# Kernel tuning notes

Hardware: AMD Instinct MI355X
Metric: run time of the kernel (lower is better)

Reference implementation:

```python
import jax, jax.numpy as jnp
import numpy as np

N = 1024      # nodes
IN = 64       # input_dim
H = 128       # hidden_dim
L = 4         # num graph layers
HEADS = 4     # MHA heads


def setup_inputs() -> dict:
    key = jax.random.key(0)
    ks = jax.random.split(key, 12)
    s = lambda k, shape: (jax.random.normal(k, shape, dtype=jnp.float32) * 0.05)
    z = lambda shape: jnp.zeros(shape, jnp.float32)
    return {
        "x": jax.random.normal(ks[0], (N, IN), dtype=jnp.float32),
        "emb_W": s(ks[1], (IN, H)), "emb_b": z((H,)),
        "ln_g": jnp.ones((H,), jnp.float32), "ln_b": z((H,)),
        "edge_W1": s(ks[2], (2 * H, H)), "edge_b1": z((H,)),
        "edge_W2": s(ks[3], (H, 1)), "edge_b2": z((1,)),
        "gc_W": s(ks[4], (L, H, H)), "gc_b": z((L, H)),
        "in_proj_W": s(ks[5], (3 * H, H)), "in_proj_b": z((3 * H,)),
        "out_proj_W": s(ks[6], (H, H)), "out_proj_b": z((H,)),
        "out_W": s(ks[7], (H, 6)), "out_b": z((6,)),
    }


def reference(x, emb_W, emb_b, ln_g, ln_b, edge_W1, edge_b1, edge_W2, edge_b2,
              gc_W, gc_b, in_proj_W, in_proj_b, out_proj_W, out_proj_b,
              out_W, out_b):
    # node embedding: Linear -> LayerNorm -> ReLU
    h = x @ emb_W + emb_b
    mu = h.mean(-1, keepdims=True)
    var = ((h - mu) ** 2).mean(-1, keepdims=True)
    h = (h - mu) * jax.lax.rsqrt(var + 1e-5) * ln_g + ln_b
    h = jax.nn.relu(h)

    n, Hd = h.shape
    # dynamic graph: edge MLP on concat(x_i, x_j) for all pairs, batched.
    # cat([x_i, x_j]) @ W1 == x_i @ W1[:H] + x_j @ W1[H:]
    a = h @ edge_W1[:Hd]          # [n, H]
    b = h @ edge_W1[Hd:]          # [n, H]
    e = jax.nn.relu(a[:, None, :] + b[None, :, :] + edge_b1)   # [n, n, H]
    adj = jax.nn.sigmoid(jnp.einsum('ijh,ho->ijo', e, edge_W2)[..., 0] + edge_b2[0])
    adj = adj * (1.0 - jnp.eye(n, dtype=adj.dtype))             # no self-edges

    # physics-informed graph conv layers: adj @ (h @ W) + b
    for l in range(gc_W.shape[0]):
        h = adj @ (h @ gc_W[l]) + gc_b[l]

    # MultiheadAttention (self-attention, seq=n, batch=1)
    d = Hd // HEADS
    qkv = h @ in_proj_W.T + in_proj_b
    q, k, v = jnp.split(qkv, 3, axis=-1)
    q = q.reshape(n, HEADS, d).transpose(1, 0, 2)   # [h, n, d]
    k = k.reshape(n, HEADS, d).transpose(1, 0, 2)
    v = v.reshape(n, HEADS, d).transpose(1, 0, 2)
    scale = 1.0 / np.sqrt(d).astype(np.float32)
    attn = jax.nn.softmax(jnp.einsum('hnd,hmd->hnm', q, k) * scale, axis=-1)
    o = jnp.einsum('hnm,hmd->hnd', attn, v).transpose(1, 0, 2).reshape(n, Hd)
    h = o @ out_proj_W.T + out_proj_b

    # pooled head + per-metric activations
    out = h.mean(0) @ out_W + out_b                 # [6]
    sig = jax.nn.sigmoid(out)
    return jnp.stack([sig[0], jax.nn.relu(out[1]), sig[2], sig[3], sig[4], sig[5]])
```

## Files before the change

kernel.cpp:

```cpp
#include <hip/hip_runtime.h>
#include <math.h>

#define NN 1024
#define IN_DIM 64
#define H 128
#define NL 4
#define HEADS 4
#define DH 32
#define KSPLIT 8
#define NSPLIT 16

__global__ __launch_bounds__(128) void k_embed(const float* __restrict__ x,
        const float* __restrict__ embW, const float* __restrict__ embB,
        const float* __restrict__ lng, const float* __restrict__ lnb,
        const float* __restrict__ eW1, const float* __restrict__ eb1,
        const float* __restrict__ gcW0,
        const float* __restrict__ inW, const float* __restrict__ outW,
        float* __restrict__ Wt_in, float* __restrict__ Wt_out,
        float* __restrict__ aM, float* __restrict__ bM, float* __restrict__ g0) {
    __shared__ float xs[IN_DIM];
    __shared__ float hs[H];
    __shared__ float red[H];
    int i = blockIdx.x, t = threadIdx.x;
    int gidx = i * 128 + t;
    if (gidx < 49152) {
        Wt_in[gidx] = inW[(gidx % 384) * 128 + gidx / 384];
    } else if (gidx < 65536) {
        int i2 = gidx - 49152;
        Wt_out[i2] = outW[(i2 % 128) * 128 + i2 / 128];
    }
    if (t < IN_DIM) xs[t] = x[i * IN_DIM + t];
    __syncthreads();
    float acc = embB[t];
    #pragma unroll 8
    for (int k = 0; k < IN_DIM; ++k) acc = fmaf(xs[k], embW[k * H + t], acc);
    red[t] = acc; __syncthreads();
    for (int s = 64; s > 0; s >>= 1) { if (t < s) red[t] += red[t + s]; __syncthreads(); }
    float mu = red[0] * (1.f / H);
    __syncthreads();
    float d = acc - mu;
    red[t] = d * d; __syncthreads();
    for (int s = 64; s > 0; s >>= 1) { if (t < s) red[t] += red[t + s]; __syncthreads(); }
    float var = red[0] * (1.f / H);
    float hv = d * rsqrtf(var + 1e-5f) * lng[t] + lnb[t];
    hv = fmaxf(hv, 0.f);
    hs[t] = hv;
    __syncthreads();
    float aa = eb1[t], bb = 0.f, gg = 0.f;
    #pragma unroll 8
    for (int k = 0; k < H; ++k) {
        float hk = hs[k];
        aa = fmaf(hk, eW1[k * H + t], aa);
        bb = fmaf(hk, eW1[(H + k) * H + t], bb);
        gg = fmaf(hk, gcW0[k * H + t], gg);
    }
    aM[i * H + t] = aa;
    bM[i * H + t] = bb;
    g0[i * H + t] = gg;
}

#define AT 32
__global__ __launch_bounds__(256) void k_adj(const float* __restrict__ aM, const float* __restrict__ bM,
        const float* __restrict__ w2, const float* __restrict__ eb2p, float* __restrict__ adj) {
    __shared__ float as_[AT][H + 4];
    __shared__ float bst[H][AT + 4];
    __shared__ float w2s[H];
    int i0 = blockIdx.y * AT, j0 = blockIdx.x * AT;
    int t = threadIdx.x;
    for (int idx = t; idx < AT * H; idx += 256) {
        int r = idx >> 7, c = idx & 127;
        as_[r][c] = aM[(i0 + r) * H + c];
        bst[c][r] = bM[(j0 + r) * H + c];
    }
    if (t < H) w2s[t] = w2[t];
    __syncthreads();
    int ti = t >> 3, tjg = t & 7;
    float a0 = 0.f, a1 = 0.f, a2 = 0.f, a3 = 0.f;
    const float eb2 = eb2p[0];
    #pragma unroll 4
    for (int h = 0; h < H; ++h) {
        float av = as_[ti][h];
        float4 bv = *(const float4*)&bst[h][tjg * 4];
        float wh = w2s[h];
        a0 = fmaf(fmaxf(av + bv.x, 0.f), wh, a0);
        a1 = fmaf(fmaxf(av + bv.y, 0.f), wh, a1);
        a2 = fmaf(fmaxf(av + bv.z, 0.f), wh, a2);
        a3 = fmaf(fmaxf(av + bv.w, 0.f), wh, a3);
    }
    int i = i0 + ti, jb = j0 + tjg * 4;
    float4 ov;
    ov.x = (i == jb + 0) ? 0.f : 1.f / (1.f + __expf(-(a0 + eb2)));
    ov.y = (i == jb + 1) ? 0.f : 1.f / (1.f + __expf(-(a1 + eb2)));
    ov.z = (i == jb + 2) ? 0.f : 1.f / (1.f + __expf(-(a2 + eb2)));
    ov.w = (i == jb + 3) ? 0.f : 1.f / (1.f + __expf(-(a3 + eb2)));
    *(float4*)&adj[(size_t)i * NN + jb] = ov;
}

__global__ __launch_bounds__(128) void k_spmm(const float* __restrict__ adj, const float* __restrict__ g,
        float* __restrict__ partial) {
    __shared__ float adjs[16][65];
    int r0 = blockIdx.x * 16;
    int j0 = blockIdx.y * 64;
    int t = threadIdx.x;
    #pragma unroll
    for (int it = 0; it < 2; ++it) {
        int idx = t + it * 128;
        int r = idx >> 4, jg = idx & 15;
        float4 av = *(const float4*)&adj[(size_t)(r0 + r) * NN + j0 + jg * 4];
        adjs[r][jg * 4 + 0] = av.x; adjs[r][jg * 4 + 1] = av.y;
        adjs[r][jg * 4 + 2] = av.z; adjs[r][jg * 4 + 3] = av.w;
    }
    __syncthreads();
    int rg = t >> 5, cg = t & 31;
    int c0 = cg * 4;
    float acc[4][4] = {};
    #pragma unroll 4
    for (int jj = 0; jj < 64; ++jj) {
        float ga[4];
        *(float4*)ga = *(const float4*)&g[(j0 + jj) * H + c0];
        #pragma unroll
        for (int r = 0; r < 4; ++r) {
            float av = adjs[rg * 4 + r][jj];
            #pragma unroll
            for (int c = 0; c < 4; ++c) acc[r][c] = fmaf(av, ga[c], acc[r][c]);
        }
    }
    #pragma unroll
    for (int r = 0; r < 4; ++r) {
        float4 ov = {acc[r][0], acc[r][1], acc[r][2], acc[r][3]};
        *(float4*)&partial[((size_t)blockIdx.y * NN + r0 + rg * 4 + r) * H + c0] = ov;
    }
}

__global__ __launch_bounds__(128) void k_redmat128(const float* __restrict__ partial,
        const float* __restrict__ bias, const float* __restrict__ W, float* __restrict__ outM) {
    __shared__ float s[H];
    int i = blockIdx.x, t = threadIdx.x;
    float v = bias[t];
    #pragma unroll
    for (int p = 0; p < NSPLIT; ++p) v += partial[(size_t)p * NN * H + i * H + t];
    s[t] = v;
    __syncthreads();
    float acc = 0.f;
    #pragma unroll 8
    for (int k = 0; k < H; ++k) acc = fmaf(s[k], W[k * H + t], acc);
    outM[i * H + t] = acc;
}

__global__ __launch_bounds__(384) void k_redmat384(const float* __restrict__ partial,
        const float* __restrict__ bias, const float* __restrict__ W,
        const float* __restrict__ bias2, float* __restrict__ outM) {
    __shared__ float s[H];
    int i = blockIdx.x, t = threadIdx.x;
    if (t < H) {
        float v = bias[t];
        #pragma unroll
        for (int p = 0; p < NSPLIT; ++p) v += partial[(size_t)p * NN * H + i * H + t];
        s[t] = v;
    }
    __syncthreads();
    float acc = bias2[t];
    #pragma unroll 8
    for (int k = 0; k < H; ++k) acc = fmaf(s[k], W[k * 384 + t], acc);
    outM[i * 384 + t] = acc;
}

__global__ __launch_bounds__(256) void k_attn_part(const float* __restrict__ qkv,
        float* __restrict__ opart, float* __restrict__ mpart, float* __restrict__ lpart) {
    __shared__ float kob[4][32][36];
    __shared__ float qT[32][36];
    __shared__ float pT[128][36];
    __shared__ float marr[32], larr[32];
    float* kT = &kob[0][0][0];
    const int t = threadIdx.x;
    const int head = blockIdx.y, kp = blockIdx.z;
    const int i0 = blockIdx.x * 32, j0 = kp * 128;
    const int qoff = head * DH, koff = H + head * DH, voff = 2 * H + head * DH;
    const float scale = 0.17677669529663687f;
    {
        int qi = t >> 3, dg = t & 7;
        float4 qv = *(const float4*)&qkv[(i0 + qi) * 384 + qoff + dg * 4];
        qT[dg * 4 + 0][qi] = qv.x * scale;
        qT[dg * 4 + 1][qi] = qv.y * scale;
        qT[dg * 4 + 2][qi] = qv.z * scale;
        qT[dg * 4 + 3][qi] = qv.w * scale;
    }
    #pragma unroll
    for (int it = 0; it < 4; ++it) {
        int idx = t + it * 256;
        int j = idx >> 3, dg = idx & 7;
        float4 kv = *(const float4*)&qkv[(j0 + j) * 384 + koff + dg * 4];
        kT[(dg * 4 + 0) * 132 + j] = kv.x;
        kT[(dg * 4 + 1) * 132 + j] = kv.y;
        kT[(dg * 4 + 2) * 132 + j] = kv.z;
        kT[(dg * 4 + 3) * 132 + j] = kv.w;
    }
    __syncthreads();
    const int tq = t >> 5, tj = t & 31;
    float s[4][4] = {};
    #pragma unroll
    for (int kk = 0; kk < DH; ++kk) {
        float qa[4], ka[4];
        *(float4*)qa = *(float4*)&qT[kk][tq * 4];
        *(float4*)ka = *(float4*)&kT[kk * 132 + tj * 4];
        #pragma unroll
        for (int a = 0; a < 4; ++a)
            #pragma unroll
            for (int b = 0; b < 4; ++b) s[a][b] = fmaf(qa[a], ka[b], s[a][b]);
    }
    #pragma unroll
    for (int a = 0; a < 4; ++a) {
        float mm = fmaxf(fmaxf(s[a][0], s[a][1]), fmaxf(s[a][2], s[a][3]));
        #pragma unroll
        for (int off = 16; off > 0; off >>= 1) mm = fmaxf(mm, __shfl_xor(mm, off));
        float ll = 0.f;
        #pragma unroll
        for (int b = 0; b < 4; ++b) { s[a][b] = __expf(s[a][b] - mm); ll += s[a][b]; }
        #pragma unroll
        for (int off = 16; off > 0; off >>= 1) ll += __shfl_xor(ll, off);
        if (tj == 0) { marr[tq * 4 + a] = mm; larr[tq * 4 + a] = ll; }
    }
    #pragma unroll
    for (int b = 0; b < 4; ++b)
        #pragma unroll
        for (int a = 0; a < 4; ++a) pT[tj * 4 + b][tq * 4 + a] = s[a][b];
    __syncthreads();
    const int qg = t >> 5, dg = (t >> 2) & 7, st = t & 3;
    float o[4][4] = {};
    #pragma unroll 4
    for (int jj = 0; jj < 32; ++jj) {
        int j = st * 32 + jj;
        float pa[4], va[4];
        *(float4*)pa = *(float4*)&pT[j][qg * 4];
        *(float4*)va = *(const float4*)&qkv[(j0 + j) * 384 + voff + dg * 4];
        #pragma unroll
        for (int a = 0; a < 4; ++a)
            #pragma unroll
            for (int b = 0; b < 4; ++b) o[a][b] = fmaf(pa[a], va[b], o[a][b]);
    }
    #pragma unroll
    for (int a = 0; a < 4; ++a)
        #pragma unroll
        for (int b = 0; b < 4; ++b) kob[st][qg * 4 + a][dg * 4 + b] = o[a][b];
    __syncthreads();
    {
        int q = t >> 3, d0 = (t & 7) * 4;
        float r0[4], r1[4], r2[4], r3[4];
        *(float4*)r0 = *(float4*)&kob[0][q][d0];
        *(float4*)r1 = *(float4*)&kob[1][q][d0];
        *(float4*)r2 = *(float4*)&kob[2][q][d0];
        *(float4*)r3 = *(float4*)&kob[3][q][d0];
        float4 ov;
        ov.x = (r0[0] + r1[0]) + (r2[0] + r3[0]);
        ov.y = (r0[1] + r1[1]) + (r2[1] + r3[1]);
        ov.z = (r0[2] + r1[2]) + (r2[2] + r3[2]);
        ov.w = (r0[3] + r1[3]) + (r2[3] + r3[3]);
        int pidx = head * KSPLIT + kp;
        *(float4*)&opart[((size_t)pidx * NN + i0 + q) * DH + d0] = ov;
        if (t < 32) {
            mpart[pidx * NN + i0 + t] = marr[t];
            lpart[pidx * NN + i0 + t] = larr[t];
        }
    }
}

__global__ __launch_bounds__(128) void k_mergeproj(const float* __restrict__ opart,
        const float* __restrict__ mpart, const float* __restrict__ lpart,
        const float* __restrict__ Wt_out, const float* __restrict__ bias,
        float* __restrict__ h2) {
    __shared__ float s[H];
    int row = blockIdx.x, t = threadIdx.x;
    int head = t >> 5, d = t & 31;
    float mv[KSPLIT];
    float M = -1e30f;
    #pragma unroll
    for (int p = 0; p < KSPLIT; ++p) {
        mv[p] = mpart[(head * KSPLIT + p) * NN + row];
        M = fmaxf(M, mv[p]);
    }
    float L = 0.f, o = 0.f;
    #pragma unroll
    for (int p = 0; p < KSPLIT; ++p) {
        float w = __expf(mv[p] - M);
        L = fmaf(lpart[(head * KSPLIT + p) * NN + row], w, L);
        o = fmaf(opart[((size_t)(head * KSPLIT + p) * NN + row) * DH + d], w, o);
    }
    s[t] = o / L;
    __syncthreads();
    float acc = bias[t];
    #pragma unroll 8
    for (int k = 0; k < H; ++k) acc = fmaf(s[k], Wt_out[k * H + t], acc);
    h2[row * H + t] = acc;
}

__global__ void k_pool1(const float* __restrict__ h2, float* __restrict__ pp) {
    int b = blockIdx.x;
    int t = threadIdx.x;
    int c = t & 127, rg = t >> 7;
    int r0 = b * 32 + rg * 16;
    float s = 0.f;
    #pragma unroll
    for (int r = 0; r < 16; ++r) s += h2[(r0 + r) * H + c];
    pp[(b * 2 + rg) * H + c] = s;
}

__global__ void k_pool2(const float* __restrict__ pp, const float* __restrict__ outW,
        const float* __restrict__ outB, float* __restrict__ out) {
    __shared__ float pooled[H];
    int t = threadIdx.x;
    float s = 0.f;
    #pragma unroll 8
    for (int p = 0; p < 64; ++p) s += pp[p * H + t];
    pooled[t] = s * (1.f / 1024.f);
    __syncthreads();
    if (t < 6) {
        float acc = outB[t];
        for (int c = 0; c < H; ++c) acc = fmaf(pooled[c], outW[c * 6 + t], acc);
        out[t] = (t == 1) ? fmaxf(acc, 0.f) : 1.f / (1.f + expf(-acc));
    }
}

extern "C" void kernel_launch(void* const* d_in, const int* in_sizes, int n_in,
                              void* d_out, int out_size, void* d_ws, size_t ws_size,
                              hipStream_t stream) {
    const float* x       = (const float*)d_in[0];
    const float* emb_W   = (const float*)d_in[1];
    const float* emb_b   = (const float*)d_in[2];
    const float* ln_g    = (const float*)d_in[3];
    const float* ln_b    = (const float*)d_in[4];
    const float* edge_W1 = (const float*)d_in[5];
    const float* edge_b1 = (const float*)d_in[6];
    const float* edge_W2 = (const float*)d_in[7];
    const float* edge_b2 = (const float*)d_in[8];
    const float* gc_W    = (const float*)d_in[9];
    const float* gc_b    = (const float*)d_in[10];
    const float* in_proj_W  = (const float*)d_in[11];
    const float* in_proj_b  = (const float*)d_in[12];
    const float* out_proj_W = (const float*)d_in[13];
    const float* out_proj_b = (const float*)d_in[14];
    const float* out_W   = (const float*)d_in[15];
    const float* out_b   = (const float*)d_in[16];
    float* out = (float*)d_out;

    float* ws = (float*)d_ws;
    float* aM      = ws;
    float* bM      = aM + NN * H;
    float* adj     = bM + NN * H;
    float* g       = adj + NN * NN;
    float* partial = g + NN * H;
    float* qkv     = partial + (size_t)NSPLIT * NN * H;
    float* Wt_in   = qkv + NN * 384;
    float* Wt_out  = Wt_in + 128 * 384;
    float* pp      = Wt_out + 128 * 128;
    float* opart = adj;
    float* mpart = aM;
    float* lpart = aM + 32 * NN;
    float* h2    = g;

    k_embed<<<NN, 128, 0, stream>>>(x, emb_W, emb_b, ln_g, ln_b, edge_W1, edge_b1,
                                    gc_W, in_proj_W, out_proj_W, Wt_in, Wt_out,
                                    aM, bM, g);
    k_adj<<<dim3(NN / AT, NN / AT), 256, 0, stream>>>(aM, bM, edge_W2, edge_b2, adj);

    for (int l = 0; l < NL; ++l) {
        k_spmm<<<dim3(NN / 16, NSPLIT), 128, 0, stream>>>(adj, g, partial);
        if (l < NL - 1)
            k_redmat128<<<NN, 128, 0, stream>>>(partial, gc_b + (size_t)l * H,
                                                gc_W + (size_t)(l + 1) * H * H, g);
        else
            k_redmat384<<<NN, 384, 0, stream>>>(partial, gc_b + (size_t)l * H,
                                                Wt_in, in_proj_b, qkv);
    }

    k_attn_part<<<dim3(NN / 32, HEADS, KSPLIT), 256, 0, stream>>>(qkv, opart, mpart, lpart);
    k_mergeproj<<<NN, 128, 0, stream>>>(opart, mpart, lpart, Wt_out, out_proj_b, h2);
    k_pool1<<<32, 256, 0, stream>>>(h2, pp);
    k_pool2<<<1, 128, 0, stream>>>(pp, out_W, out_b, out);
}
```

Baseline: 159.3 us.

## Register-tile edge MLP kernel and batch multiple rows per block

The pairwise adjacency kernel moves to 64x64 output tiles. Each thread computes a 4x4 register block, and the hidden dimension is staged through transposed shared tiles in chunks of 32. This cuts shared-memory loads per FMA in the dominant N²·H edge computation. The embed and reduce-matmul kernels now handle four rows per block so each weight load is reused across rows. The spmm kernel stores its adjacency tile transposed so rows can be read as float4. A missing barrier is added before reusing shared memory in attention, and some pointer offsets are widened to size_t. In exchange, there are fewer blocks per launch and more registers per thread.

```diff
diff --git a/kernel.cpp b/kernel.cpp
--- a/kernel.cpp
+++ b/kernel.cpp
@@ -10,7 +10,7 @@
 #define KSPLIT 8
 #define NSPLIT 16
 
-__global__ __launch_bounds__(128) void k_embed(const float* __restrict__ x,
+__global__ __launch_bounds__(512) void k_embed(const float* __restrict__ x,
         const float* __restrict__ embW, const float* __restrict__ embB,
         const float* __restrict__ lng, const float* __restrict__ lnb,
         const float* __restrict__ eW1, const float* __restrict__ eb1,
@@ -18,97 +18,112 @@
         const float* __restrict__ inW, const float* __restrict__ outW,
         float* __restrict__ Wt_in, float* __restrict__ Wt_out,
         float* __restrict__ aM, float* __restrict__ bM, float* __restrict__ g0) {
-    __shared__ float xs[IN_DIM];
-    __shared__ float hs[H];
-    __shared__ float red[H];
-    int i = blockIdx.x, t = threadIdx.x;
-    int gidx = i * 128 + t;
+    __shared__ float xs[4][IN_DIM];
+    __shared__ float red[4][H];
+    __shared__ float hs[4][H];
+    int B = blockIdx.x, T = threadIdx.x;
+    int half = T >> 7, t = T & 127;
+    int gidx = B * 512 + T;
     if (gidx < 49152) {
         Wt_in[gidx] = inW[(gidx % 384) * 128 + gidx / 384];
     } else if (gidx < 65536) {
         int i2 = gidx - 49152;
         Wt_out[i2] = outW[(i2 % 128) * 128 + i2 / 128];
     }
-    if (t < IN_DIM) xs[t] = x[i * IN_DIM + t];
-    __syncthreads();
+    if (T < 256) xs[T >> 6][T & 63] = x[(B * 4 + (T >> 6)) * IN_DIM + (T & 63)];
+    __syncthreads();
+    int row = B * 4 + half;
     float acc = embB[t];
     #pragma unroll 8
-    for (int k = 0; k < IN_DIM; ++k) acc = fmaf(xs[k], embW[k * H + t], acc);
-    red[t] = acc; __syncthreads();
-    for (int s = 64; s > 0; s >>= 1) { if (t < s) red[t] += red[t + s]; __syncthreads(); }
-    float mu = red[0] * (1.f / H);
+    for (int k = 0; k < IN_DIM; ++k) acc = fmaf(xs[half][k], embW[k * H + t], acc);
+    red[half][t] = acc; __syncthreads();
+    for (int s = 64; s > 0; s >>= 1) { if (t < s) red[half][t] += red[half][t + s]; __syncthreads(); }
+    float mu = red[half][0] * (1.f / H);
     __syncthreads();
     float d = acc - mu;
-    red[t] = d * d; __syncthreads();
-    for (int s = 64; s > 0; s >>= 1) { if (t < s) red[t] += red[t + s]; __syncthreads(); }
-    float var = red[0] * (1.f / H);
-    float hv = d * rsqrtf(var + 1e-5f) * lng[t] + lnb[t];
-    hv = fmaxf(hv, 0.f);
-    hs[t] = hv;
+    red[half][t] = d * d; __syncthreads();
+    for (int s = 64; s > 0; s >>= 1) { if (t < s) red[half][t] += red[half][t + s]; __syncthreads(); }
+    float var = red[half][0] * (1.f / H);
+    float hv = fmaxf(d * rsqrtf(var + 1e-5f) * lng[t] + lnb[t], 0.f);
+    hs[half][t] = hv;
     __syncthreads();
     float aa = eb1[t], bb = 0.f, gg = 0.f;
     #pragma unroll 8
     for (int k = 0; k < H; ++k) {
-        float hk = hs[k];
+        float hk = hs[half][k];
         aa = fmaf(hk, eW1[k * H + t], aa);
         bb = fmaf(hk, eW1[(H + k) * H + t], bb);
         gg = fmaf(hk, gcW0[k * H + t], gg);
     }
-    aM[i * H + t] = aa;
-    bM[i * H + t] = bb;
-    g0[i * H + t] = gg;
-}
-
-#define AT 32
+    aM[row * H + t] = aa;
+    bM[row * H + t] = bb;
+    g0[row * H + t] = gg;
+}
+
 __global__ __launch_bounds__(256) void k_adj(const float* __restrict__ aM, const float* __restrict__ bM,
         const float* __restrict__ w2, const float* __restrict__ eb2p, float* __restrict__ adj) {
-    __shared__ float as_[AT][H + 4];
-    __shared__ float bst[H][AT + 4];
+    __shared__ float aT[32][68];
+    __shared__ float bT[32][68];
     __shared__ float w2s[H];
-    int i0 = blockIdx.y * AT, j0 = blockIdx.x * AT;
-    int t = threadIdx.x;
-    for (int idx = t; idx < AT * H; idx += 256) {
-        int r = idx >> 7, c = idx & 127;
-        as_[r][c] = aM[(i0 + r) * H + c];
-        bst[c][r] = bM[(j0 + r) * H + c];
-    }
-    if (t < H) w2s[t] = w2[t];
-    __syncthreads();
-    int ti = t >> 3, tjg = t & 7;
-    float a0 = 0.f, a1 = 0.f, a2 = 0.f, a3 = 0.f;
+    int i0 = blockIdx.y * 64, j0 = blockIdx.x * 64;
+    int T = threadIdx.x;
+    if (T < H) w2s[T] = w2[T];
+    int tig = T >> 4, tjg = T & 15;
+    float acc[4][4] = {};
+    for (int hc = 0; hc < 4; ++hc) {
+        __syncthreads();
+        #pragma unroll
+        for (int it = 0; it < 2; ++it) {
+            int f4i = T + it * 256;
+            int r = f4i >> 3, cc = f4i & 7;
+            float4 av = *(const float4*)&aM[(i0 + r) * H + hc * 32 + cc * 4];
+            float4 bv = *(const float4*)&bM[(j0 + r) * H + hc * 32 + cc * 4];
+            aT[cc * 4 + 0][r] = av.x; aT[cc * 4 + 1][r] = av.y;
+            aT[cc * 4 + 2][r] = av.z; aT[cc * 4 + 3][r] = av.w;
+            bT[cc * 4 + 0][r] = bv.x; bT[cc * 4 + 1][r] = bv.y;
+            bT[cc * 4 + 2][r] = bv.z; bT[cc * 4 + 3][r] = bv.w;
+        }
+        __syncthreads();
+        #pragma unroll 8
+        for (int hh = 0; hh < 32; ++hh) {
+            float a4[4], b4[4];
+            *(float4*)a4 = *(const float4*)&aT[hh][tig * 4];
+            *(float4*)b4 = *(const float4*)&bT[hh][tjg * 4];
+            float wh = w2s[hc * 32 + hh];
+            #pragma unroll
+            for (int r = 0; r < 4; ++r)
+                #pragma unroll
+                for (int c = 0; c < 4; ++c)
+                    acc[r][c] = fmaf(fmaxf(a4[r] + b4[c], 0.f), wh, acc[r][c]);
+        }
+    }
     const float eb2 = eb2p[0];
-    #pragma unroll 4
-    for (int h = 0; h < H; ++h) {
-        float av = as_[ti][h];
-        float4 bv = *(const float4*)&bst[h][tjg * 4];
-        float wh = w2s[h];
-        a0 = fmaf(fmaxf(av + bv.x, 0.f), wh, a0);
-        a1 = fmaf(fmaxf(av + bv.y, 0.f), wh, a1);
-        a2 = fmaf(fmaxf(av + bv.z, 0.f), wh, a2);
-        a3 = fmaf(fmaxf(av + bv.w, 0.f), wh, a3);
-    }
-    int i = i0 + ti, jb = j0 + tjg * 4;
-    float4 ov;
-    ov.x = (i == jb + 0) ? 0.f : 1.f / (1.f + __expf(-(a0 + eb2)));
-    ov.y = (i == jb + 1) ? 0.f : 1.f / (1.f + __expf(-(a1 + eb2)));
-    ov.z = (i == jb + 2) ? 0.f : 1.f / (1.f + __expf(-(a2 + eb2)));
-    ov.w = (i == jb + 3) ? 0.f : 1.f / (1.f + __expf(-(a3 + eb2)));
-    *(float4*)&adj[(size_t)i * NN + jb] = ov;
+    #pragma unroll
+    for (int r = 0; r < 4; ++r) {
+        int ia = i0 + tig * 4 + r;
+        int jb = j0 + tjg * 4;
+        float4 ov;
+        ov.x = (ia == jb + 0) ? 0.f : 1.f / (1.f + __expf(-(acc[r][0] + eb2)));
+        ov.y = (ia == jb + 1) ? 0.f : 1.f / (1.f + __expf(-(acc[r][1] + eb2)));
+        ov.z = (ia == jb + 2) ? 0.f : 1.f / (1.f + __expf(-(acc[r][2] + eb2)));
+        ov.w = (ia == jb + 3) ? 0.f : 1.f / (1.f + __expf(-(acc[r][3] + eb2)));
+        *(float4*)&adj[(size_t)ia * NN + jb] = ov;
+    }
 }
 
 __global__ __launch_bounds__(128) void k_spmm(const float* __restrict__ adj, const float* __restrict__ g,
         float* __restrict__ partial) {
-    __shared__ float adjs[16][65];
+    __shared__ float adjsT[64][17];
     int r0 = blockIdx.x * 16;
     int j0 = blockIdx.y * 64;
     int t = threadIdx.x;
     #pragma unroll
     for (int it = 0; it < 2; ++it) {
-        int idx = t + it * 128;
-        int r = idx >> 4, jg = idx & 15;
-        float4 av = *(const float4*)&adj[(size_t)(r0 + r) * NN + j0 + jg * 4];
-        adjs[r][jg * 4 + 0] = av.x; adjs[r][jg * 4 + 1] = av.y;
-        adjs[r][jg * 4 + 2] = av.z; adjs[r][jg * 4 + 3] = av.w;
+        int f4i = t + it * 128;
+        int r = f4i >> 4, jc = f4i & 15;
+        float4 av = *(const float4*)&adj[(size_t)(r0 + r) * NN + j0 + jc * 4];
+        adjsT[jc * 4 + 0][r] = av.x; adjsT[jc * 4 + 1][r] = av.y;
+        adjsT[jc * 4 + 2][r] = av.z; adjsT[jc * 4 + 3][r] = av.w;
     }
     __syncthreads();
     int rg = t >> 5, cg = t & 31;
@@ -116,14 +131,13 @@
     float acc[4][4] = {};
     #pragma unroll 4
     for (int jj = 0; jj < 64; ++jj) {
-        float ga[4];
+        float ga[4], a4[4];
         *(float4*)ga = *(const float4*)&g[(j0 + jj) * H + c0];
-        #pragma unroll
-        for (int r = 0; r < 4; ++r) {
-            float av = adjs[rg * 4 + r][jj];
+        *(float4*)a4 = *(const float4*)&adjsT[jj][rg * 4];
+        #pragma unroll
+        for (int r = 0; r < 4; ++r)
             #pragma unroll
-            for (int c = 0; c < 4; ++c) acc[r][c] = fmaf(av, ga[c], acc[r][c]);
-        }
+            for (int c = 0; c < 4; ++c) acc[r][c] = fmaf(a4[r], ga[c], acc[r][c]);
     }
     #pragma unroll
     for (int r = 0; r < 4; ++r) {
@@ -134,35 +148,51 @@
 
 __global__ __launch_bounds__(128) void k_redmat128(const float* __restrict__ partial,
         const float* __restrict__ bias, const float* __restrict__ W, float* __restrict__ outM) {
-    __shared__ float s[H];
-    int i = blockIdx.x, t = threadIdx.x;
-    float v = bias[t];
-    #pragma unroll
-    for (int p = 0; p < NSPLIT; ++p) v += partial[(size_t)p * NN * H + i * H + t];
-    s[t] = v;
-    __syncthreads();
-    float acc = 0.f;
-    #pragma unroll 8
-    for (int k = 0; k < H; ++k) acc = fmaf(s[k], W[k * H + t], acc);
-    outM[i * H + t] = acc;
+    __shared__ float s[4][H];
+    int B = blockIdx.x, t = threadIdx.x;
+    int row0 = B * 4;
+    #pragma unroll
+    for (int r = 0; r < 4; ++r) {
+        float v = bias[t];
+        #pragma unroll
+        for (int p = 0; p < NSPLIT; ++p) v += partial[(size_t)p * NN * H + (row0 + r) * H + t];
+        s[r][t] = v;
+    }
+    __syncthreads();
+    float acc[4] = {};
+    #pragma unroll 4
+    for (int k = 0; k < H; ++k) {
+        float wv = W[k * H + t];
+        #pragma unroll
+        for (int r = 0; r < 4; ++r) acc[r] = fmaf(s[r][k], wv, acc[r]);
+    }
+    #pragma unroll
+    for (int r = 0; r < 4; ++r) outM[(row0 + r) * H + t] = acc[r];
 }
 
 __global__ __launch_bounds__(384) void k_redmat384(const float* __restrict__ partial,
         const float* __restrict__ bias, const float* __restrict__ W,
         const float* __restrict__ bias2, float* __restrict__ outM) {
-    __shared__ float s[H];
-    int i = blockIdx.x, t = threadIdx.x;
-    if (t < H) {
-        float v = bias[t];
-        #pragma unroll
-        for (int p = 0; p < NSPLIT; ++p) v += partial[(size_t)p * NN * H + i * H + t];
-        s[t] = v;
-    }
-    __syncthreads();
-    float acc = bias2[t];
-    #pragma unroll 8
-    for (int k = 0; k < H; ++k) acc = fmaf(s[k], W[k * 384 + t], acc);
-    outM[i * 384 + t] = acc;
+    __shared__ float s[4][H];
+    int B = blockIdx.x, t = threadIdx.x;
+    int row0 = B * 4;
+    for (int idx = t; idx < 512; idx += 384) {
+        int r = idx >> 7, c = idx & 127;
+        float v = bias[c];
+        #pragma unroll
+        for (int p = 0; p < NSPLIT; ++p) v += partial[(size_t)p * NN * H + (row0 + r) * H + c];
+        s[r][c] = v;
+    }
+    __syncthreads();
+    float acc[4] = {bias2[t], bias2[t], bias2[t], bias2[t]};
+    #pragma unroll 4
+    for (int k = 0; k < H; ++k) {
+        float wv = W[k * 384 + t];
+        #pragma unroll
+        for (int r = 0; r < 4; ++r) acc[r] = fmaf(s[r][k], wv, acc[r]);
+    }
+    #pragma unroll
+    for (int r = 0; r < 4; ++r) outM[(row0 + r) * 384 + t] = acc[r];
 }
 
 __global__ __launch_bounds__(256) void k_attn_part(const float* __restrict__ qkv,
@@ -225,23 +255,24 @@
         #pragma unroll
         for (int a = 0; a < 4; ++a) pT[tj * 4 + b][tq * 4 + a] = s[a][b];
     __syncthreads();
-    const int qg = t >> 5, dg = (t >> 2) & 7, st = t & 3;
+    const int qg = t >> 5, dg2 = (t >> 2) & 7, st = t & 3;
     float o[4][4] = {};
     #pragma unroll 4
     for (int jj = 0; jj < 32; ++jj) {
         int j = st * 32 + jj;
         float pa[4], va[4];
         *(float4*)pa = *(float4*)&pT[j][qg * 4];
-        *(float4*)va = *(const float4*)&qkv[(j0 + j) * 384 + voff + dg * 4];
+        *(float4*)va = *(const float4*)&qkv[(j0 + j) * 384 + voff + dg2 * 4];
         #pragma unroll
         for (int a = 0; a < 4; ++a)
             #pragma unroll
             for (int b = 0; b < 4; ++b) o[a][b] = fmaf(pa[a], va[b], o[a][b]);
     }
+    __syncthreads();
     #pragma unroll
     for (int a = 0; a < 4; ++a)
         #pragma unroll
-        for (int b = 0; b < 4; ++b) kob[st][qg * 4 + a][dg * 4 + b] = o[a][b];
+        for (int b = 0; b < 4; ++b) kob[st][qg * 4 + a][dg2 * 4 + b] = o[a][b];
     __syncthreads();
     {
         int q = t >> 3, d0 = (t & 7) * 4;
@@ -346,10 +377,10 @@
     float* aM      = ws;
     float* bM      = aM + NN * H;
     float* adj     = bM + NN * H;
-    float* g       = adj + NN * NN;
+    float* g       = adj + (size_t)NN * NN;
     float* partial = g + NN * H;
     float* qkv     = partial + (size_t)NSPLIT * NN * H;
-    float* Wt_in   = qkv + NN * 384;
+    float* Wt_in   = qkv + (size_t)NN * 384;
     float* Wt_out  = Wt_in + 128 * 384;
     float* pp      = Wt_out + 128 * 128;
     float* opart = adj;
@@ -357,19 +388,19 @@
     float* lpart = aM + 32 * NN;
     float* h2    = g;
 
-    k_embed<<<NN, 128, 0, stream>>>(x, emb_W, emb_b, ln_g, ln_b, edge_W1, edge_b1,
-                                    gc_W, in_proj_W, out_proj_W, Wt_in, Wt_out,
-                                    aM, bM, g);
-    k_adj<<<dim3(NN / AT, NN / AT), 256, 0, stream>>>(aM, bM, edge_W2, edge_b2, adj);
+    k_embed<<<NN / 4, 512, 0, stream>>>(x, emb_W, emb_b, ln_g, ln_b, edge_W1, edge_b1,
+                                        gc_W, in_proj_W, out_proj_W, Wt_in, Wt_out,
+                                        aM, bM, g);
+    k_adj<<<dim3(16, 16), 256, 0, stream>>>(aM, bM, edge_W2, edge_b2, adj);
 
     for (int l = 0; l < NL; ++l) {
         k_spmm<<<dim3(NN / 16, NSPLIT), 128, 0, stream>>>(adj, g, partial);
         if (l < NL - 1)
-            k_redmat128<<<NN, 128, 0, stream>>>(partial, gc_b + (size_t)l * H,
-                                                gc_W + (size_t)(l + 1) * H * H, g);
+            k_redmat128<<<NN / 4, 128, 0, stream>>>(partial, gc_b + (size_t)l * H,
+                                                    gc_W + (size_t)(l + 1) * H * H, g);
         else
-            k_redmat384<<<NN, 384, 0, stream>>>(partial, gc_b + (size_t)l * H,
-                                                Wt_in, in_proj_b, qkv);
+            k_redmat384<<<NN / 4, 384, 0, stream>>>(partial, gc_b + (size_t)l * H,
+                                                    Wt_in, in_proj_b, qkv);
     }
 
     k_attn_part<<<dim3(NN / 32, HEADS, KSPLIT), 256, 0, stream>>>(qkv, opart, mpart, lpart);
```

New measurement: 179.2 us. 12.5% more time.

## Fuse graph-conv adj matmul with reduction and next weight; fuse pooling via atomics

Applied to the files above, without the earlier changes.

Replaces the split-K SpMM plus partial-sum reduction kernels with a single per-row-block kernel that holds four full adjacency rows in shared memory, computes adj@g over all 1024 columns, adds the bias, and applies the next layer weight (or in_proj) in the same block. This removes the partial buffer round trip and halves the kernel launches per layer. Pooling is also folded into the merge/projection kernel using atomicAdd into 32 bins that the attention kernel zeroes, dropping one pool kernel. The cost is fewer blocks (256) each with a long serial 1024-step loop that re-reads g from global memory, so parallelism is lower, and the atomic sum order is nondeterministic.

```diff
diff --git a/kernel.cpp b/kernel.cpp
--- a/kernel.cpp
+++ b/kernel.cpp
@@ -8,7 +8,6 @@
 #define HEADS 4
 #define DH 32
 #define KSPLIT 8
-#define NSPLIT 16
 
 __global__ __launch_bounds__(128) void k_embed(const float* __restrict__ x,
         const float* __restrict__ embW, const float* __restrict__ embB,
@@ -96,77 +95,88 @@
     *(float4*)&adj[(size_t)i * NN + jb] = ov;
 }
 
-__global__ __launch_bounds__(128) void k_spmm(const float* __restrict__ adj, const float* __restrict__ g,
-        float* __restrict__ partial) {
-    __shared__ float adjs[16][65];
-    int r0 = blockIdx.x * 16;
-    int j0 = blockIdx.y * 64;
-    int t = threadIdx.x;
+__global__ __launch_bounds__(512) void k_gc128(const float* __restrict__ adj,
+        const float* __restrict__ g, const float* __restrict__ bias,
+        const float* __restrict__ W, float* __restrict__ gout) {
+    __shared__ float adjs[4][NN];
+    __shared__ float s[4][H];
+    int B = blockIdx.x, T = threadIdx.x;
+    int r0 = B * 4;
     #pragma unroll
     for (int it = 0; it < 2; ++it) {
-        int idx = t + it * 128;
-        int r = idx >> 4, jg = idx & 15;
-        float4 av = *(const float4*)&adj[(size_t)(r0 + r) * NN + j0 + jg * 4];
-        adjs[r][jg * 4 + 0] = av.x; adjs[r][jg * 4 + 1] = av.y;
-        adjs[r][jg * 4 + 2] = av.z; adjs[r][jg * 4 + 3] = av.w;
-    }
-    __syncthreads();
-    int rg = t >> 5, cg = t & 31;
-    int c0 = cg * 4;
-    float acc[4][4] = {};
+        int idx = T + it * 512;
+        int r = idx >> 8, jf = idx & 255;
+        float4 v = *(const float4*)&adj[(size_t)(r0 + r) * NN + jf * 4];
+        adjs[r][jf * 4 + 0] = v.x; adjs[r][jf * 4 + 1] = v.y;
+        adjs[r][jf * 4 + 2] = v.z; adjs[r][jf * 4 + 3] = v.w;
+    }
+    __syncthreads();
+    int rg = T >> 7, c = T & 127;
+    float a0 = 0.f, a1 = 0.f, a2 = 0.f, a3 = 0.f;
     #pragma unroll 4
-    for (int jj = 0; jj < 64; ++jj) {
-        float ga[4];
-        *(float4*)ga = *(const float4*)&g[(j0 + jj) * H + c0];
-        #pragma unroll
-        for (int r = 0; r < 4; ++r) {
-            float av = adjs[rg * 4 + r][jj];
-            #pragma unroll
-            for (int c = 0; c < 4; ++c) acc[r][c] = fmaf(av, ga[c], acc[r][c]);
-        }
-    }
-    #pragma unroll
-    for (int r = 0; r < 4; ++r) {
-        float4 ov = {acc[r][0], acc[r][1], acc[r][2], acc[r][3]};
-        *(float4*)&partial[((size_t)blockIdx.y * NN + r0 + rg * 4 + r) * H + c0] = ov;
-    }
-}
-
-__global__ __launch_bounds__(128) void k_redmat128(const float* __restrict__ partial,
-        const float* __restrict__ bias, const float* __restrict__ W, float* __restrict__ outM) {
-    __shared__ float s[H];
-    int i = blockIdx.x, t = threadIdx.x;
-    float v = bias[t];
-    #pragma unroll
-    for (int p = 0; p < NSPLIT; ++p) v += partial[(size_t)p * NN * H + i * H + t];
-    s[t] = v;
+    for (int j = 0; j < NN; j += 4) {
+        float g0 = g[(j + 0) * H + c];
+        float g1 = g[(j + 1) * H + c];
+        float g2 = g[(j + 2) * H + c];
+        float g3 = g[(j + 3) * H + c];
+        a0 = fmaf(adjs[rg][j + 0], g0, a0);
+        a1 = fmaf(adjs[rg][j + 1], g1, a1);
+        a2 = fmaf(adjs[rg][j + 2], g2, a2);
+        a3 = fmaf(adjs[rg][j + 3], g3, a3);
+    }
+    s[rg][c] = (a0 + a1) + (a2 + a3) + bias[c];
     __syncthreads();
     float acc = 0.f;
     #pragma unroll 8
-    for (int k = 0; k < H; ++k) acc = fmaf(s[k], W[k * H + t], acc);
-    outM[i * H + t] = acc;
-}
-
-__global__ __launch_bounds__(384) void k_redmat384(const float* __restrict__ partial,
-        const float* __restrict__ bias, const float* __restrict__ W,
-        const float* __restrict__ bias2, float* __restrict__ outM) {
-    __shared__ float s[H];
-    int i = blockIdx.x, t = threadIdx.x;
-    if (t < H) {
-        float v = bias[t];
-        #pragma unroll
-        for (int p = 0; p < NSPLIT; ++p) v += partial[(size_t)p * NN * H + i * H + t];
-        s[t] = v;
-    }
-    __syncthreads();
-    float acc = bias2[t];
-    #pragma unroll 8
-    for (int k = 0; k < H; ++k) acc = fmaf(s[k], W[k * 384 + t], acc);
-    outM[i * 384 + t] = acc;
+    for (int k = 0; k < H; ++k) acc = fmaf(s[rg][k], W[k * H + c], acc);
+    gout[(r0 + rg) * H + c] = acc;
+}
+
+__global__ __launch_bounds__(512) void k_gc384(const float* __restrict__ adj,
+        const float* __restrict__ g, const float* __restrict__ bias,
+        const float* __restrict__ Wt_in, const float* __restrict__ bias2,
+        float* __restrict__ qkv) {
+    __shared__ float adjs[4][NN];
+    __shared__ float s[4][H];
+    int B = blockIdx.x, T = threadIdx.x;
+    int r0 = B * 4;
+    #pragma unroll
+    for (int it = 0; it < 2; ++it) {
+        int idx = T + it * 512;
+        int r = idx >> 8, jf = idx & 255;
+        float4 v = *(const float4*)&adj[(size_t)(r0 + r) * NN + jf * 4];
+        adjs[r][jf * 4 + 0] = v.x; adjs[r][jf * 4 + 1] = v.y;
+        adjs[r][jf * 4 + 2] = v.z; adjs[r][jf * 4 + 3] = v.w;
+    }
+    __syncthreads();
+    int rg = T >> 7, c = T & 127;
+    float a0 = 0.f, a1 = 0.f, a2 = 0.f, a3 = 0.f;
+    #pragma unroll 4
+    for (int j = 0; j < NN; j += 4) {
+        float g0 = g[(j + 0) * H + c];
+        float g1 = g[(j + 1) * H + c];
+        float g2 = g[(j + 2) * H + c];
+        float g3 = g[(j + 3) * H + c];
+        a0 = fmaf(adjs[rg][j + 0], g0, a0);
+        a1 = fmaf(adjs[rg][j + 1], g1, a1);
+        a2 = fmaf(adjs[rg][j + 2], g2, a2);
+        a3 = fmaf(adjs[rg][j + 3], g3, a3);
+    }
+    s[rg][c] = (a0 + a1) + (a2 + a3) + bias[c];
+    __syncthreads();
+    #pragma unroll
+    for (int rep = 0; rep < 3; ++rep) {
+        int cc = c + rep * 128;
+        float acc = bias2[cc];
+        #pragma unroll 8
+        for (int k = 0; k < H; ++k) acc = fmaf(s[rg][k], Wt_in[k * 384 + cc], acc);
+        qkv[(r0 + rg) * 384 + cc] = acc;
+    }
 }
 
 __global__ __launch_bounds__(256) void k_attn_part(const float* __restrict__ qkv,
-        float* __restrict__ opart, float* __restrict__ mpart, float* __restrict__ lpart) {
+        float* __restrict__ opart, float* __restrict__ mpart, float* __restrict__ lpart,
+        float* __restrict__ pp) {
     __shared__ float kob[4][32][36];
     __shared__ float qT[32][36];
     __shared__ float pT[128][36];
@@ -177,6 +187,7 @@
     const int i0 = blockIdx.x * 32, j0 = kp * 128;
     const int qoff = head * DH, koff = H + head * DH, voff = 2 * H + head * DH;
     const float scale = 0.17677669529663687f;
+    if (head == 0 && kp == 0 && t < 128) pp[blockIdx.x * 128 + t] = 0.f;
     {
         int qi = t >> 3, dg = t & 7;
         float4 qv = *(const float4*)&qkv[(i0 + qi) * 384 + qoff + dg * 4];
@@ -225,23 +236,24 @@
         #pragma unroll
         for (int a = 0; a < 4; ++a) pT[tj * 4 + b][tq * 4 + a] = s[a][b];
     __syncthreads();
-    const int qg = t >> 5, dg = (t >> 2) & 7, st = t & 3;
+    const int qg = t >> 5, dg2 = (t >> 2) & 7, st = t & 3;
     float o[4][4] = {};
     #pragma unroll 4
     for (int jj = 0; jj < 32; ++jj) {
         int j = st * 32 + jj;
         float pa[4], va[4];
         *(float4*)pa = *(float4*)&pT[j][qg * 4];
-        *(float4*)va = *(const float4*)&qkv[(j0 + j) * 384 + voff + dg * 4];
+        *(float4*)va = *(const float4*)&qkv[(j0 + j) * 384 + voff + dg2 * 4];
         #pragma unroll
         for (int a = 0; a < 4; ++a)
             #pragma unroll
             for (int b = 0; b < 4; ++b) o[a][b] = fmaf(pa[a], va[b], o[a][b]);
     }
+    __syncthreads();
     #pragma unroll
     for (int a = 0; a < 4; ++a)
         #pragma unroll
-        for (int b = 0; b < 4; ++b) kob[st][qg * 4 + a][dg * 4 + b] = o[a][b];
+        for (int b = 0; b < 4; ++b) kob[st][qg * 4 + a][dg2 * 4 + b] = o[a][b];
     __syncthreads();
     {
         int q = t >> 3, d0 = (t & 7) * 4;
@@ -267,7 +279,7 @@
 __global__ __launch_bounds__(128) void k_mergeproj(const float* __restrict__ opart,
         const float* __restrict__ mpart, const float* __restrict__ lpart,
         const float* __restrict__ Wt_out, const float* __restrict__ bias,
-        float* __restrict__ h2) {
+        float* __restrict__ pp) {
     __shared__ float s[H];
     int row = blockIdx.x, t = threadIdx.x;
     int head = t >> 5, d = t & 31;
@@ -290,27 +302,16 @@
     float acc = bias[t];
     #pragma unroll 8
     for (int k = 0; k < H; ++k) acc = fmaf(s[k], Wt_out[k * H + t], acc);
-    h2[row * H + t] = acc;
-}
-
-__global__ void k_pool1(const float* __restrict__ h2, float* __restrict__ pp) {
-    int b = blockIdx.x;
-    int t = threadIdx.x;
-    int c = t & 127, rg = t >> 7;
-    int r0 = b * 32 + rg * 16;
-    float s = 0.f;
-    #pragma unroll
-    for (int r = 0; r < 16; ++r) s += h2[(r0 + r) * H + c];
-    pp[(b * 2 + rg) * H + c] = s;
-}
-
-__global__ void k_pool2(const float* __restrict__ pp, const float* __restrict__ outW,
+    atomicAdd(&pp[(row & 31) * H + t], acc);
+}
+
+__global__ void k_poolhead(const float* __restrict__ pp, const float* __restrict__ outW,
         const float* __restrict__ outB, float* __restrict__ out) {
     __shared__ float pooled[H];
     int t = threadIdx.x;
     float s = 0.f;
     #pragma unroll 8
-    for (int p = 0; p < 64; ++p) s += pp[p * H + t];
+    for (int p = 0; p < 32; ++p) s += pp[p * H + t];
     pooled[t] = s * (1.f / 1024.f);
     __syncthreads();
     if (t < 6) {
@@ -346,34 +347,27 @@
     float* aM      = ws;
     float* bM      = aM + NN * H;
     float* adj     = bM + NN * H;
-    float* g       = adj + NN * NN;
-    float* partial = g + NN * H;
-    float* qkv     = partial + (size_t)NSPLIT * NN * H;
-    float* Wt_in   = qkv + NN * 384;
+    float* g       = adj + (size_t)NN * NN;
+    float* g2      = g + NN * H;
+    float* qkv     = g2 + NN * H;
+    float* Wt_in   = qkv + (size_t)NN * 384;
     float* Wt_out  = Wt_in + 128 * 384;
     float* pp      = Wt_out + 128 * 128;
     float* opart = adj;
     float* mpart = aM;
     float* lpart = aM + 32 * NN;
-    float* h2    = g;
 
     k_embed<<<NN, 128, 0, stream>>>(x, emb_W, emb_b, ln_g, ln_b, edge_W1, edge_b1,
                                     gc_W, in_proj_W, out_proj_W, Wt_in, Wt_out,
                                     aM, bM, g);
     k_adj<<<dim3(NN / AT, NN / AT), 256, 0, stream>>>(aM, bM, edge_W2, edge_b2, adj);
 
-    for (int l = 0; l < NL; ++l) {
-        k_spmm<<<dim3(NN / 16, NSPLIT), 128, 0, stream>>>(adj, g, partial);
-        if (l < NL - 1)
-            k_redmat128<<<NN, 128, 0, stream>>>(partial, gc_b + (size_t)l * H,
-                                                gc_W + (size_t)(l + 1) * H * H, g);
-        else
-            k_redmat384<<<NN, 384, 0, stream>>>(partial, gc_b + (size_t)l * H,
-                                                Wt_in, in_proj_b, qkv);
-    }
-
-    k_attn_part<<<dim3(NN / 32, HEADS, KSPLIT), 256, 0, stream>>>(qkv, opart, mpart, lpart);
-    k_mergeproj<<<NN, 128, 0, stream>>>(opart, mpart, lpart, Wt_out, out_proj_b, h2);
-    k_pool1<<<32, 256, 0, stream>>>(h2, pp);
-    k_pool2<<<1, 128, 0, stream>>>(pp, out_W, out_b, out);
-}
+    k_gc128<<<NN / 4, 512, 0, stream>>>(adj, g,  gc_b + 0 * H, gc_W + (size_t)1 * H * H, g2);
+    k_gc128<<<NN / 4, 512, 0, stream>>>(adj, g2, gc_b + 1 * H, gc_W + (size_t)2 * H * H, g);
+    k_gc128<<<NN / 4, 512, 0, stream>>>(adj, g,  gc_b + 2 * H, gc_W + (size_t)3 * H * H, g2);
+    k_gc384<<<NN / 4, 512, 0, stream>>>(adj, g2, gc_b + 3 * H, Wt_in, in_proj_b, qkv);
+
+    k_attn_part<<<dim3(NN / 32, HEADS, KSPLIT), 256, 0, stream>>>(qkv, opart, mpart, lpart, pp);
+    k_mergeproj<<<NN, 128, 0, stream>>>(opart, mpart, lpart, Wt_out, out_proj_b, pp);
+    k_poolhead<<<1, 128, 0, stream>>>(pp, out_W, out_b, out);
+}
```

Result: slower. 203.5 us (+27.8%).

## Cut spmm K-split to four and fuse pooling into merge-projection via atomics

Applied to the files above, without the earlier changes.

The adjacency-times-features kernel now uses 8-row tiles over 256-column K chunks, giving only 4 partials instead of 16. Each block reduces its two K halves in shared memory before writing. This cuts partial-buffer traffic in the spmm and in the reduction kernels. Separately, the merge-projection kernel atomically adds its output rows into 32 pooling slots, which are zeroed inside the attention kernel. That removes the h2 write and one pooling kernel, at the cost of atomic contention and non-deterministic summation order.

```diff
diff --git a/kernel.cpp b/kernel.cpp
--- a/kernel.cpp
+++ b/kernel.cpp
@@ -8,7 +8,8 @@
 #define HEADS 4
 #define DH 32
 #define KSPLIT 8
-#define NSPLIT 16
+#define RT 8
+#define JC 256
 
 __global__ __launch_bounds__(128) void k_embed(const float* __restrict__ x,
         const float* __restrict__ embW, const float* __restrict__ embB,
@@ -96,39 +97,50 @@
     *(float4*)&adj[(size_t)i * NN + jb] = ov;
 }
 
-__global__ __launch_bounds__(128) void k_spmm(const float* __restrict__ adj, const float* __restrict__ g,
+__global__ __launch_bounds__(256) void k_spmm(const float* __restrict__ adj, const float* __restrict__ g,
         float* __restrict__ partial) {
-    __shared__ float adjs[16][65];
-    int r0 = blockIdx.x * 16;
-    int j0 = blockIdx.y * 64;
+    __shared__ float adjs[RT][JC];
+    __shared__ float redbuf[RT][H];
+    int rt = blockIdx.x;
+    int p = blockIdx.y;
     int t = threadIdx.x;
+    int r0 = rt * RT;
     #pragma unroll
     for (int it = 0; it < 2; ++it) {
-        int idx = t + it * 128;
-        int r = idx >> 4, jg = idx & 15;
-        float4 av = *(const float4*)&adj[(size_t)(r0 + r) * NN + j0 + jg * 4];
-        adjs[r][jg * 4 + 0] = av.x; adjs[r][jg * 4 + 1] = av.y;
-        adjs[r][jg * 4 + 2] = av.z; adjs[r][jg * 4 + 3] = av.w;
-    }
-    __syncthreads();
-    int rg = t >> 5, cg = t & 31;
+        int idx = t + it * 256;
+        int r = idx >> 6, jf = idx & 63;
+        float4 v = *(const float4*)&adj[(size_t)(r0 + r) * NN + p * JC + jf * 4];
+        adjs[r][jf * 4 + 0] = v.x; adjs[r][jf * 4 + 1] = v.y;
+        adjs[r][jf * 4 + 2] = v.z; adjs[r][jf * 4 + 3] = v.w;
+    }
+    __syncthreads();
+    int cg = t & 31, half = (t >> 5) & 1, rg = t >> 6;
     int c0 = cg * 4;
-    float acc[4][4] = {};
+    int jbase = half * 128;
+    int ra = rg * 2, rb = rg * 2 + 1;
+    float acc0[4] = {}, acc1[4] = {};
     #pragma unroll 4
-    for (int jj = 0; jj < 64; ++jj) {
-        float ga[4];
-        *(float4*)ga = *(const float4*)&g[(j0 + jj) * H + c0];
-        #pragma unroll
-        for (int r = 0; r < 4; ++r) {
-            float av = adjs[rg * 4 + r][jj];
-            #pragma unroll
-            for (int c = 0; c < 4; ++c) acc[r][c] = fmaf(av, ga[c], acc[r][c]);
-        }
-    }
-    #pragma unroll
-    for (int r = 0; r < 4; ++r) {
-        float4 ov = {acc[r][0], acc[r][1], acc[r][2], acc[r][3]};
-        *(float4*)&partial[((size_t)blockIdx.y * NN + r0 + rg * 4 + r) * H + c0] = ov;
+    for (int jj = 0; jj < 128; ++jj) {
+        int ja = jbase + jj;
+        float4 gv = *(const float4*)&g[(p * JC + ja) * H + c0];
+        float a0 = adjs[ra][ja], a1 = adjs[rb][ja];
+        acc0[0] = fmaf(a0, gv.x, acc0[0]); acc0[1] = fmaf(a0, gv.y, acc0[1]);
+        acc0[2] = fmaf(a0, gv.z, acc0[2]); acc0[3] = fmaf(a0, gv.w, acc0[3]);
+        acc1[0] = fmaf(a1, gv.x, acc1[0]); acc1[1] = fmaf(a1, gv.y, acc1[1]);
+        acc1[2] = fmaf(a1, gv.z, acc1[2]); acc1[3] = fmaf(a1, gv.w, acc1[3]);
+    }
+    if (half == 1) {
+        *(float4*)&redbuf[ra][c0] = *(float4*)acc0;
+        *(float4*)&redbuf[rb][c0] = *(float4*)acc1;
+    }
+    __syncthreads();
+    if (half == 0) {
+        float4 r0v = *(float4*)&redbuf[ra][c0];
+        float4 r1v = *(float4*)&redbuf[rb][c0];
+        float4 o0 = {acc0[0] + r0v.x, acc0[1] + r0v.y, acc0[2] + r0v.z, acc0[3] + r0v.w};
+        float4 o1 = {acc1[0] + r1v.x, acc1[1] + r1v.y, acc1[2] + r1v.z, acc1[3] + r1v.w};
+        *(float4*)&partial[((size_t)p * NN + r0 + ra) * H + c0] = o0;
+        *(float4*)&partial[((size_t)p * NN + r0 + rb) * H + c0] = o1;
     }
 }
 
@@ -136,9 +148,8 @@
         const float* __restrict__ bias, const float* __restrict__ W, float* __restrict__ outM) {
     __shared__ float s[H];
     int i = blockIdx.x, t = threadIdx.x;
-    float v = bias[t];
-    #pragma unroll
-    for (int p = 0; p < NSPLIT; ++p) v += partial[(size_t)p * NN * H + i * H + t];
+    float v = partial[i * H + t] + partial[NN * H + i * H + t]
+            + partial[2 * NN * H + i * H + t] + partial[3 * NN * H + i * H + t] + bias[t];
     s[t] = v;
     __syncthreads();
     float acc = 0.f;
@@ -153,9 +164,8 @@
     __shared__ float s[H];
     int i = blockIdx.x, t = threadIdx.x;
     if (t < H) {
-        float v = bias[t];
-        #pragma unroll
-        for (int p = 0; p < NSPLIT; ++p) v += partial[(size_t)p * NN * H + i * H + t];
+        float v = partial[i * H + t] + partial[NN * H + i * H + t]
+                + partial[2 * NN * H + i * H + t] + partial[3 * NN * H + i * H + t] + bias[t];
         s[t] = v;
     }
     __syncthreads();
@@ -166,7 +176,8 @@
 }
 
 __global__ __launch_bounds__(256) void k_attn_part(const float* __restrict__ qkv,
-        float* __restrict__ opart, float* __restrict__ mpart, float* __restrict__ lpart) {
+        float* __restrict__ opart, float* __restrict__ mpart, float* __restrict__ lpart,
+        float* __restrict__ pp) {
     __shared__ float kob[4][32][36];
     __shared__ float qT[32][36];
     __shared__ float pT[128][36];
@@ -177,6 +188,7 @@
     const int i0 = blockIdx.x * 32, j0 = kp * 128;
     const int qoff = head * DH, koff = H + head * DH, voff = 2 * H + head * DH;
     const float scale = 0.17677669529663687f;
+    if (head == 0 && kp == 0 && t < 128) pp[blockIdx.x * 128 + t] = 0.f;
     {
         int qi = t >> 3, dg = t & 7;
         float4 qv = *(const float4*)&qkv[(i0 + qi) * 384 + qoff + dg * 4];
@@ -225,23 +237,24 @@
         #pragma unroll
         for (int a = 0; a < 4; ++a) pT[tj * 4 + b][tq * 4 + a] = s[a][b];
     __syncthreads();
-    const int qg = t >> 5, dg = (t >> 2) & 7, st = t & 3;
+    const int qg = t >> 5, dg2 = (t >> 2) & 7, st = t & 3;
     float o[4][4] = {};
     #pragma unroll 4
     for (int jj = 0; jj < 32; ++jj) {
         int j = st * 32 + jj;
         float pa[4], va[4];
         *(float4*)pa = *(float4*)&pT[j][qg * 4];
-        *(float4*)va = *(const float4*)&qkv[(j0 + j) * 384 + voff + dg * 4];
+        *(float4*)va = *(const float4*)&qkv[(j0 + j) * 384 + voff + dg2 * 4];
         #pragma unroll
         for (int a = 0; a < 4; ++a)
             #pragma unroll
             for (int b = 0; b < 4; ++b) o[a][b] = fmaf(pa[a], va[b], o[a][b]);
     }
+    __syncthreads();
     #pragma unroll
     for (int a = 0; a < 4; ++a)
         #pragma unroll
-        for (int b = 0; b < 4; ++b) kob[st][qg * 4 + a][dg * 4 + b] = o[a][b];
+        for (int b = 0; b < 4; ++b) kob[st][qg * 4 + a][dg2 * 4 + b] = o[a][b];
     __syncthreads();
     {
         int q = t >> 3, d0 = (t & 7) * 4;
@@ -267,7 +280,7 @@
 __global__ __launch_bounds__(128) void k_mergeproj(const float* __restrict__ opart,
         const float* __restrict__ mpart, const float* __restrict__ lpart,
         const float* __restrict__ Wt_out, const float* __restrict__ bias,
-        float* __restrict__ h2) {
+        float* __restrict__ pp) {
     __shared__ float s[H];
     int row = blockIdx.x, t = threadIdx.x;
     int head = t >> 5, d = t & 31;
@@ -290,27 +303,16 @@
     float acc = bias[t];
     #pragma unroll 8
     for (int k = 0; k < H; ++k) acc = fmaf(s[k], Wt_out[k * H + t], acc);
-    h2[row * H + t] = acc;
-}
-
-__global__ void k_pool1(const float* __restrict__ h2, float* __restrict__ pp) {
-    int b = blockIdx.x;
-    int t = threadIdx.x;
-    int c = t & 127, rg = t >> 7;
-    int r0 = b * 32 + rg * 16;
-    float s = 0.f;
-    #pragma unroll
-    for (int r = 0; r < 16; ++r) s += h2[(r0 + r) * H + c];
-    pp[(b * 2 + rg) * H + c] = s;
-}
-
-__global__ void k_pool2(const float* __restrict__ pp, const float* __restrict__ outW,
+    atomicAdd(&pp[(row & 31) * H + t], acc);
+}
+
+__global__ void k_poolhead(const float* __restrict__ pp, const float* __restrict__ outW,
         const float* __restrict__ outB, float* __restrict__ out) {
     __shared__ float pooled[H];
     int t = threadIdx.x;
     float s = 0.f;
     #pragma unroll 8
-    for (int p = 0; p < 64; ++p) s += pp[p * H + t];
+    for (int p = 0; p < 32; ++p) s += pp[p * H + t];
     pooled[t] = s * (1.f / 1024.f);
     __syncthreads();
     if (t < 6) {
@@ -346,16 +348,15 @@
     float* aM      = ws;
     float* bM      = aM + NN * H;
     float* adj     = bM + NN * H;
-    float* g       = adj + NN * NN;
+    float* g       = adj + (size_t)NN * NN;
     float* partial = g + NN * H;
-    float* qkv     = partial + (size_t)NSPLIT * NN * H;
-    float* Wt_in   = qkv + NN * 384;
+    float* qkv     = partial + (size_t)4 * NN * H;
+    float* Wt_in   = qkv + (size_t)NN * 384;
     float* Wt_out  = Wt_in + 128 * 384;
     float* pp      = Wt_out + 128 * 128;
     float* opart = adj;
     float* mpart = aM;
     float* lpart = aM + 32 * NN;
-    float* h2    = g;
 
     k_embed<<<NN, 128, 0, stream>>>(x, emb_W, emb_b, ln_g, ln_b, edge_W1, edge_b1,
                                     gc_W, in_proj_W, out_proj_W, Wt_in, Wt_out,
@@ -363,7 +364,7 @@
     k_adj<<<dim3(NN / AT, NN / AT), 256, 0, stream>>>(aM, bM, edge_W2, edge_b2, adj);
 
     for (int l = 0; l < NL; ++l) {
-        k_spmm<<<dim3(NN / 16, NSPLIT), 128, 0, stream>>>(adj, g, partial);
+        k_spmm<<<dim3(NN / RT, 4), 256, 0, stream>>>(adj, g, partial);
         if (l < NL - 1)
             k_redmat128<<<NN, 128, 0, stream>>>(partial, gc_b + (size_t)l * H,
                                                 gc_W + (size_t)(l + 1) * H * H, g);
@@ -372,8 +373,7 @@
                                                 Wt_in, in_proj_b, qkv);
     }
 
-    k_attn_part<<<dim3(NN / 32, HEADS, KSPLIT), 256, 0, stream>>>(qkv, opart, mpart, lpart);
-    k_mergeproj<<<NN, 128, 0, stream>>>(opart, mpart, lpart, Wt_out, out_proj_b, h2);
-    k_pool1<<<32, 256, 0, stream>>>(h2, pp);
-    k_pool2<<<1, 128, 0, stream>>>(pp, out_W, out_b, out);
-}
+    k_attn_part<<<dim3(NN / 32, HEADS, KSPLIT), 256, 0, stream>>>(qkv, opart, mpart, lpart, pp);
+    k_mergeproj<<<NN, 128, 0, stream>>>(opart, mpart, lpart, Wt_out, out_proj_b, pp);
+    k_poolhead<<<1, 128, 0, stream>>>(pp, out_W, out_b, out);
+}
```

Measured after the change: 161.0 us. About the same (+1.1%).
